# Performance work log

Measured on AMD Instinct MI355X. Metric: run time of the kernel, lower is better.

## Reference

```python
import jax, jax.numpy as jnp
import numpy as np

N = 4096        # nodes
E = 65536       # edges (avg degree 16)
L = 64          # latent_dims
K = 256         # kernel_dims
ED = 6          # edge_dims
DEPTH = 2


def _gelu(x):
    # torch.nn.GELU / F.gelu default = exact erf form
    return jax.nn.gelu(x, approximate=False)


def setup_inputs() -> dict:
    key = jax.random.key(0)
    ks = jax.random.split(key, 12)
    u = lambda k, shape, fan: jax.random.uniform(k, shape, jnp.float32, -1.0, 1.0) / np.sqrt(fan)
    return {
        "nodes": jax.random.normal(ks[0], (N, L), jnp.float32),
        "edge_index": jax.random.randint(ks[1], (2, E), 0, N, jnp.int32),
        "edge_attr": jax.random.uniform(ks[2], (E, ED), jnp.float32),
        # DenseNet kernel MLP: ED -> K -> K -> L*L (GELU between layers)
        "W1": u(ks[3], (ED, K), ED), "b1": jnp.zeros((K,), jnp.float32),
        "W2": u(ks[4], (K, K), K),  "b2": jnp.zeros((K,), jnp.float32),
        "W3": u(ks[5], (K, L * L), K), "b3": jnp.zeros((L * L,), jnp.float32),
        # NNConv root linear (no bias) + conv bias
        "W_root": u(ks[6], (L, L), L),
        "bias": jnp.zeros((L,), jnp.float32),
    }


def reference(nodes, edge_index, edge_attr, W1, b1, W2, b2, W3, b3, W_root, bias):
    src, dst = edge_index[0], edge_index[1]
    # Edge-conditioned dynamic weights (depend only on edge_attr -> compute once)
    h = _gelu(edge_attr @ W1 + b1)          # [E, K]
    h = _gelu(h @ W2 + b2)                  # [E, K]
    W_edge = (h @ W3 + b3).reshape(E, L, L) # [E, L_in, L_out]

    def conv(x):
        msg = jnp.einsum('ei,eio->eo', x[src], W_edge)          # gather + per-edge matmul
        agg = jax.ops.segment_sum(msg, dst, num_segments=N)     # scatter-add to dst
        return agg + x @ W_root + bias

    x = nodes
    for idx in range(DEPTH):
        x = conv(x)
        if idx < DEPTH - 1:
            x = _gelu(x)
    return x
```

## Files before the change

### kernel.cpp

```cpp
#include <hip/hip_runtime.h>
#include <math.h>

#define NN 4096
#define NE 65536
#define LL 64
#define KK 256
#define ED 6
#define MAXSUPER 6144

typedef __bf16 bf16_t;
typedef __attribute__((ext_vector_type(4))) __bf16 bf16x4;
typedef __attribute__((ext_vector_type(8))) __bf16 bf16x8;
typedef __attribute__((ext_vector_type(4))) float f32x4;
typedef __attribute__((ext_vector_type(16))) float f32x16;

#define OFF_CNT    ((size_t)0)
#define OFF_DESC   ((size_t)16384)
#define OFF_AGG0   ((size_t)147456)
#define OFF_AGG1   ((size_t)1196032)
#define ZERO_BYTES ((size_t)2244608)
#define OFF_CURSOR ((size_t)2244608)
#define OFF_DSTS   ((size_t)2260992)
#define OFF_W2R    ((size_t)2785280)
#define OFF_W3RR   ((size_t)2916352)
#define OFF_Q0     ((size_t)5013504)
#define OFF_Q1     ((size_t)6062080)
#define OFF_X1F    ((size_t)7110656)
#define OFF_X0BF   ((size_t)8159232)
#define OFF_X1BF   ((size_t)8683520)
#define OFF_H      ((size_t)9207808)
#define OFF_P      ((size_t)42762240)

__device__ __forceinline__ float gelu_f(float x) {
    return 0.5f * x * (1.0f + erff(x * 0.7071067811865476f));
}
__device__ __forceinline__ bf16_t f2bf(float x) { return (bf16_t)x; }

__global__ void k_hist(const int* __restrict__ ei, int* __restrict__ cnt) {
    int e = blockIdx.x * 256 + threadIdx.x;
    atomicAdd(&cnt[ei[e]], 1);
}

__global__ void k_scan(const int* __restrict__ cnt, int* __restrict__ cursor,
                       int4* __restrict__ descs) {
    __shared__ int pd[1024], pc[1024];
    int t = threadIdx.x;
    int deg[4]; int sd = 0, sc = 0;
#pragma unroll
    for (int j = 0; j < 4; j++) {
        deg[j] = cnt[t * 4 + j];
        sd += deg[j];
        sc += (deg[j] + 31) >> 5;
    }
    pd[t] = sd; pc[t] = sc;
    __syncthreads();
    for (int off = 1; off < 1024; off <<= 1) {
        int vd = 0, vc = 0;
        if (t >= off) { vd = pd[t - off]; vc = pc[t - off]; }
        __syncthreads();
        pd[t] += vd; pc[t] += vc;
        __syncthreads();
    }
    int rd = (t > 0) ? pd[t - 1] : 0;
    int rc = (t > 0) ? pc[t - 1] : 0;
    for (int j = 0; j < 4; j++) {
        int v = t * 4 + j, d = deg[j];
        cursor[v] = rd;
        int nch = (d + 31) >> 5;
        for (int c = 0; c < nch; c++) {
            int rem = d - c * 32;
            descs[rc + c] = make_int4(v, rd + c * 32, rem < 32 ? rem : 32, 0);
        }
        rc += nch; rd += d;
    }
}

__global__ void __launch_bounds__(256) k_fuse3(
        const int* __restrict__ ei, int* __restrict__ cursor, int* __restrict__ dsts,
        const float* __restrict__ W3, bf16_t* __restrict__ W3rr,
        const float* __restrict__ W2, bf16_t* __restrict__ W2r,
        const float* __restrict__ attr, const float* __restrict__ W1,
        const float* __restrict__ b1, bf16_t* __restrict__ a1,
        const float* __restrict__ x, const float* __restrict__ b3,
        bf16_t* __restrict__ xbf, float* __restrict__ Q) {
    __shared__ float smem[4096];
    int bid = blockIdx.x, tid = threadIdx.x;
    if (bid < 256) {
        int k0 = bid;
        for (int idx = tid; idx < 4096; idx += 256)
            smem[idx] = W3[(size_t)k0 * 4096 + idx];
        __syncthreads();
        int sbase = (2 * (k0 >> 4)) * 512 + (((k0 >> 3) & 1) * 32) * 8 + (k0 & 7);
#pragma unroll
        for (int m = 0; m < 2; m++) {
            int w = m * 256 + tid;
            int o = w >> 3, ib = w & 7;
            int s = sbase + (o >> 5) * 512 + (o & 31) * 8;
            int f = (s >> 4) * 1024 + (ib >> 2) * 512 + (ib & 3) * 128 + (s & 15) * 8;
            bf16x8 pk;
#pragma unroll
            for (int j = 0; j < 8; j++) pk[j] = f2bf(smem[(ib * 8 + j) * 64 + o]);
            *(bf16x8*)(W3rr + f) = pk;
        }
    } else if (bid < 512) {
        int t = (bid - 256) * 256 + tid;
        int kk = t >> 13, nn = (t >> 9) & 15, lane = (t >> 3) & 63, j = t & 7;
        int k = kk * 32 + (lane >> 4) * 8 + j;
        int n = nn * 16 + (lane & 15);
        W2r[t] = f2bf(W2[k * 256 + n]);
    } else if (bid < 1536) {
        float* sa = smem;
        int* spos = (int*)(smem + 512);
        int e0 = (bid - 512) * 64;
        for (int i = tid; i < 64 * ED; i += 256) sa[i] = attr[(size_t)e0 * ED + i];
        if (tid < 64) {
            int e = e0 + tid;
            int s = ei[e], d = ei[NE + e];
            int p = atomicAdd(&cursor[s], 1);
            dsts[p] = d;
            spos[tid] = p;
        }
        int col4 = (tid & 63) * 4;
        float w[ED][4], bb[4];
#pragma unroll
        for (int j = 0; j < ED; j++)
#pragma unroll
            for (int c = 0; c < 4; c++) w[j][c] = W1[j * 256 + col4 + c];
#pragma unroll
        for (int c = 0; c < 4; c++) bb[c] = b1[col4 + c];
        __syncthreads();
        int esub = tid >> 6;
#pragma unroll 1
        for (int eg = 0; eg < 16; eg++) {
            int el = eg * 4 + esub;
            int pos = spos[el];
            float av[ED];
#pragma unroll
            for (int j = 0; j < ED; j++) av[j] = sa[el * ED + j];
            bf16x4 ov;
#pragma unroll
            for (int c = 0; c < 4; c++) {
                float acc = bb[c];
#pragma unroll
                for (int j = 0; j < ED; j++) acc += av[j] * w[j][c];
                ov[c] = f2bf(gelu_f(acc));
            }
            *(bf16x4*)(a1 + (size_t)pos * 256 + col4) = ov;
        }
    } else {
        int v = (bid - 1536) * 4 + (tid >> 6);
        int o = tid & 63;
        float xv = x[v * 64 + o];
        smem[tid] = xv;
        xbf[v * 64 + o] = f2bf(xv);
        __syncthreads();
        const float* sx = smem + (tid >> 6) * 64;
        float q = 0.0f;
#pragma unroll 8
        for (int i = 0; i < 64; i++) q += sx[i] * b3[i * 64 + o];
        Q[v * 64 + o] = q;
    }
}

__device__ __forceinline__ void pgemm_body(const bf16_t* __restrict__ xbf,
                                           const bf16_t* __restrict__ W3rr,
                                           bf16_t* __restrict__ P,
                                           bf16_t* __restrict__ sw_wave,
                                           int strip, int rg) {
    int wave = threadIdx.x >> 6, lane = threadIdx.x & 63;
    int col = lane & 15, quad = lane >> 4;
    int half = lane >> 5, l5 = lane & 31;
    bf16_t* sw = sw_wave + wave * 4224;
    bf16x8 b[16][2];
#pragma unroll
    for (int nn = 0; nn < 16; nn++) {
        int sn = strip * 16 + nn;
#pragma unroll
        for (int ki = 0; ki < 2; ki++)
            b[nn][ki] = *(const bf16x8*)(W3rr + (size_t)(sn * 2 + ki) * 512 + lane * 8);
    }
#pragma unroll 1
    for (int rt = 0; rt < 4; rt++) {
        int rowbase = rg * 256 + wave * 64 + rt * 16;
        const bf16_t* arow = xbf + (size_t)(rowbase + col) * 64;
        bf16x8 a0 = *(const bf16x8*)(arow + quad * 8);
        bf16x8 a1v = *(const bf16x8*)(arow + 32 + quad * 8);
#pragma unroll
        for (int nn = 0; nn < 16; nn++) {
            f32x4 acc;
#pragma unroll
            for (int r = 0; r < 4; r++) acc[r] = 0.0f;
            acc = __builtin_amdgcn_mfma_f32_16x16x32_bf16(b[nn][0], a0, acc, 0, 0, 0);
            acc = __builtin_amdgcn_mfma_f32_16x16x32_bf16(b[nn][1], a1v, acc, 0, 0, 0);
            bf16x4 pk;
#pragma unroll
            for (int r = 0; r < 4; r++) pk[r] = f2bf(acc[r]);
            *(bf16x4*)(sw + col * 264 + nn * 16 + quad * 4) = pk;
        }
        __builtin_amdgcn_wave_barrier();
#pragma unroll
        for (int i = 0; i < 8; i++) {
            int r2 = 2 * i + half;
            int vrow = rowbase + r2;
            bf16x8 vb = *(const bf16x8*)(sw + r2 * 264 + l5 * 8);
            *(bf16x8*)(P + ((size_t)strip * 4096 + vrow) * 256 + l5 * 8) = vb;
        }
        __builtin_amdgcn_wave_barrier();
    }
}

__global__ void __launch_bounds__(256) k_fuse4(const bf16_t* __restrict__ xbf,
                                               const bf16_t* __restrict__ W3rr,
                                               bf16_t* __restrict__ P,
                                               const bf16_t* a1,
                                               const bf16_t* __restrict__ W2r,
                                               const float* __restrict__ b2,
                                               bf16_t* h) {
    __shared__ bf16_t sB[16896];
    if (blockIdx.x < 1024) {
        pgemm_body(xbf, W3rr, P, sB, blockIdx.x & 63, blockIdx.x >> 6);
    } else {
        int tid = threadIdx.x;
        int wave = tid >> 6, lane = tid & 63, col = lane & 15, quad = lane >> 4;
        int base = (blockIdx.x - 1024) * 128 + wave * 32;
        bf16x8 a[2][8];
#pragma unroll
        for (int t = 0; t < 2; t++) {
            const bf16_t* arow = a1 + (size_t)(base + t * 16 + col) * 256;
#pragma unroll
            for (int kk = 0; kk < 8; kk++)
                a[t][kk] = *(const bf16x8*)(arow + kk * 32 + quad * 8);
        }
#pragma unroll 1
        for (int p = 0; p < 4; p++) {
#pragma unroll
            for (int it = 0; it < 8; it++) {
                int c = it * 256 + tid;
                int fl = c >> 6;
                int e = (c & 63) * 8;
                int kk = fl >> 2, nnl = fl & 3;
                *(bf16x8*)(sB + fl * 512 + e) =
                    *(const bf16x8*)(W2r + (size_t)(kk * 16 + p * 4 + nnl) * 512 + e);
            }
            __syncthreads();
#pragma unroll
            for (int nnl = 0; nnl < 4; nnl++) {
                f32x4 acc0, acc1;
#pragma unroll
                for (int r = 0; r < 4; r++) { acc0[r] = 0.0f; acc1[r] = 0.0f; }
#pragma unroll
                for (int kk = 0; kk < 8; kk++) {
                    bf16x8 b = *(const bf16x8*)(sB + (kk * 4 + nnl) * 512 + lane * 8);
                    acc0 = __builtin_amdgcn_mfma_f32_16x16x32_bf16(a[0][kk], b, acc0, 0, 0, 0);
                    acc1 = __builtin_amdgcn_mfma_f32_16x16x32_bf16(a[1][kk], b, acc1, 0, 0, 0);
                }
                int ncol = (p * 4 + nnl) * 16 + col;
                float bv = b2[ncol];
#pragma unroll
                for (int r = 0; r < 4; r++) {
                    int row0 = base + quad * 4 + r;
                    h[(size_t)row0 * 256 + ncol] = f2bf(gelu_f(acc0[r] + bv));
                    h[(size_t)(row0 + 16) * 256 + ncol] = f2bf(gelu_f(acc1[r] + bv));
                }
            }
            __syncthreads();
        }
    }
}

__global__ void __launch_bounds__(256) k_pgemm(const bf16_t* __restrict__ xbf,
                                               const bf16_t* __restrict__ W3rr,
                                               bf16_t* __restrict__ P) {
    __shared__ bf16_t sw_all[16896];
    pgemm_body(xbf, W3rr, P, sw_all, blockIdx.x & 63, blockIdx.x >> 6);
}

__global__ void __launch_bounds__(256) k_agg(const int4* __restrict__ descs,
                                             const int* __restrict__ dsts,
                                             const bf16_t* __restrict__ h,
                                             const bf16_t* __restrict__ P,
                                             const float* __restrict__ Q,
                                             float* __restrict__ agg) {
    int chunk = blockIdx.x * 4 + (threadIdx.x >> 6);
    int lane = threadIdx.x & 63;
    int row = lane & 31, khalf = lane >> 5;
    int4 d = descs[chunk];
    int v = d.x, base = d.y, cnt = d.z;
    if (cnt == 0) return;
    bool valid = (row < cnt);
    int pos = base + (valid ? row : 0);
    int dst = dsts[pos];

    bf16x8 zero;
#pragma unroll
    for (int i = 0; i < 8; i++) zero[i] = (bf16_t)0.0f;

    bf16x8 a[16];
    const bf16_t* hrow = h + (size_t)pos * 256;
#pragma unroll
    for (int kt = 0; kt < 16; kt++) {
        bf16x8 t = *(const bf16x8*)(hrow + kt * 16 + khalf * 8);
        a[kt] = valid ? t : zero;
    }
    const bf16_t* Pv = P + ((size_t)khalf * 4096 + v) * 256 + row * 8;
    f32x16 acc0, acc1;
#pragma unroll
    for (int r = 0; r < 16; r++) { acc0[r] = 0.0f; acc1[r] = 0.0f; }
#pragma unroll
    for (int kt = 0; kt < 16; kt++) {
        bf16x8 b0 = *(const bf16x8*)(Pv + (size_t)(4 * kt) * 4096 * 256);
        bf16x8 b1 = *(const bf16x8*)(Pv + (size_t)(4 * kt + 2) * 4096 * 256);
        acc0 = __builtin_amdgcn_mfma_f32_32x32x16_bf16(a[kt], b0, acc0, 0, 0, 0);
        acc1 = __builtin_amdgcn_mfma_f32_32x32x16_bf16(a[kt], b1, acc1, 0, 0, 0);
    }
    float q0 = Q[v * 64 + row];
    float q1 = Q[v * 64 + 32 + row];
#pragma unroll
    for (int r = 0; r < 16; r++) {
        int mm = (r & 3) + 8 * (r >> 2) + 4 * khalf;
        int de = __shfl(dst, mm, 64);
        if (mm < cnt) {
            atomicAdd(&agg[(size_t)de * 64 + row], acc0[r] + q0);
            atomicAdd(&agg[(size_t)de * 64 + 32 + row], acc1[r] + q1);
        }
    }
}

__global__ void k_combine1(const float* __restrict__ x, const float* __restrict__ agg,
                           const float* __restrict__ Wroot, const float* __restrict__ bias,
                           const float* __restrict__ b3, float* __restrict__ x1,
                           bf16_t* __restrict__ x1bf, float* __restrict__ Q1) {
    __shared__ float sx[64], sy[64];
    int v = blockIdx.x, o = threadIdx.x;
    sx[o] = x[v * 64 + o];
    __syncthreads();
    float acc = agg[v * 64 + o] + bias[o];
#pragma unroll 8
    for (int i = 0; i < 64; i++) acc += sx[i] * Wroot[i * 64 + o];
    acc = gelu_f(acc);
    x1[v * 64 + o] = acc;
    x1bf[v * 64 + o] = f2bf(acc);
    sy[o] = acc;
    __syncthreads();
    float q = 0.0f;
#pragma unroll 8
    for (int i = 0; i < 64; i++) q += sy[i] * b3[i * 64 + o];
    Q1[v * 64 + o] = q;
}

__global__ void k_combine2(const float* __restrict__ x1, const float* __restrict__ agg,
                           const float* __restrict__ Wroot, const float* __restrict__ bias,
                           float* __restrict__ out) {
    __shared__ float sx[64];
    int v = blockIdx.x, o = threadIdx.x;
    sx[o] = x1[v * 64 + o];
    __syncthreads();
    float acc = agg[v * 64 + o] + bias[o];
#pragma unroll 8
    for (int i = 0; i < 64; i++) acc += sx[i] * Wroot[i * 64 + o];
    out[v * 64 + o] = acc;
}

extern "C" void kernel_launch(void* const* d_in, const int* in_sizes, int n_in,
                              void* d_out, int out_size, void* d_ws, size_t ws_size,
                              hipStream_t stream) {
    const float* nodes = (const float*)d_in[0];
    const int*   ei    = (const int*)d_in[1];
    const float* attr  = (const float*)d_in[2];
    const float* W1    = (const float*)d_in[3];
    const float* b1    = (const float*)d_in[4];
    const float* W2    = (const float*)d_in[5];
    const float* b2    = (const float*)d_in[6];
    const float* W3    = (const float*)d_in[7];
    const float* b3    = (const float*)d_in[8];
    const float* Wroot = (const float*)d_in[9];
    const float* bias  = (const float*)d_in[10];
    float* out = (float*)d_out;
    char* ws = (char*)d_ws;

    int*    cnt    = (int*)(ws + OFF_CNT);
    int4*   descs  = (int4*)(ws + OFF_DESC);
    float*  agg0   = (float*)(ws + OFF_AGG0);
    float*  agg1   = (float*)(ws + OFF_AGG1);
    int*    cursor = (int*)(ws + OFF_CURSOR);
    int*    dsts   = (int*)(ws + OFF_DSTS);
    bf16_t* W2r    = (bf16_t*)(ws + OFF_W2R);
    bf16_t* W3rr   = (bf16_t*)(ws + OFF_W3RR);
    float*  Q0     = (float*)(ws + OFF_Q0);
    float*  Q1     = (float*)(ws + OFF_Q1);
    float*  x1f    = (float*)(ws + OFF_X1F);
    bf16_t* x0bf   = (bf16_t*)(ws + OFF_X0BF);
    bf16_t* x1bf   = (bf16_t*)(ws + OFF_X1BF);
    bf16_t* hbuf   = (bf16_t*)(ws + OFF_H);
    bf16_t* a1buf  = (bf16_t*)(ws + OFF_H);
    bf16_t* Pbuf   = (bf16_t*)(ws + OFF_P);

    hipMemsetAsync(ws, 0, ZERO_BYTES, stream);
    k_hist<<<NE / 256, 256, 0, stream>>>(ei, cnt);
    k_scan<<<1, 1024, 0, stream>>>(cnt, cursor, descs);
    k_fuse3<<<2560, 256, 0, stream>>>(ei, cursor, dsts, W3, W3rr, W2, W2r,
                                      attr, W1, b1, a1buf, nodes, b3, x0bf, Q0);
    k_fuse4<<<1536, 256, 0, stream>>>(x0bf, W3rr, Pbuf, a1buf, W2r, b2, hbuf);
    k_agg<<<MAXSUPER / 4, 256, 0, stream>>>(descs, dsts, hbuf, Pbuf, Q0, agg0);
    k_combine1<<<NN, 64, 0, stream>>>(nodes, agg0, Wroot, bias, b3, x1f, x1bf, Q1);
    k_pgemm<<<1024, 256, 0, stream>>>(x1bf, W3rr, Pbuf);
    k_agg<<<MAXSUPER / 4, 256, 0, stream>>>(descs, dsts, hbuf, Pbuf, Q1, agg1);
    k_combine2<<<NN, 64, 0, stream>>>(x1f, agg1, Wroot, bias, out);
}
```

Before: 262.4 us.

## Fuse per-node P projection into aggregation kernel, dropping global P buffer

Instead of materializing the per-node projection P = x·W3 (4096×64×256 bf16) to global memory in a separate kernel and reading it back in the aggregation, the new aggregation kernel computes P for its 16 source nodes on the fly into LDS, then immediately runs the edge MFMA against h. The MLP second layer becomes a standalone kernel. This removes a large global write and read of P per layer, in exchange for recomputing P per chunk (nodes split across multiple chunks recompute) and adding block-wide barriers per k-step.

```diff
diff --git a/kernel.cpp b/kernel.cpp
--- a/kernel.cpp
+++ b/kernel.cpp
@@ -29,7 +29,6 @@
 #define OFF_X0BF   ((size_t)8159232)
 #define OFF_X1BF   ((size_t)8683520)
 #define OFF_H      ((size_t)9207808)
-#define OFF_P      ((size_t)42762240)
 
 __device__ __forceinline__ float gelu_f(float x) {
     return 0.5f * x * (1.0f + erff(x * 0.7071067811865476f));
@@ -162,166 +161,166 @@
     }
 }
 
-__device__ __forceinline__ void pgemm_body(const bf16_t* __restrict__ xbf,
-                                           const bf16_t* __restrict__ W3rr,
-                                           bf16_t* __restrict__ P,
-                                           bf16_t* __restrict__ sw_wave,
-                                           int strip, int rg) {
-    int wave = threadIdx.x >> 6, lane = threadIdx.x & 63;
+__global__ void __launch_bounds__(256) k_mlp2(const bf16_t* a1,
+                                              const bf16_t* __restrict__ W2r,
+                                              const float* __restrict__ b2,
+                                              bf16_t* h) {
+    __shared__ bf16_t sB[16384];
+    int tid = threadIdx.x;
+    int wave = tid >> 6, lane = tid & 63, col = lane & 15, quad = lane >> 4;
+    int base = blockIdx.x * 128 + wave * 32;
+    bf16x8 a[2][8];
+#pragma unroll
+    for (int t = 0; t < 2; t++) {
+        const bf16_t* arow = a1 + (size_t)(base + t * 16 + col) * 256;
+#pragma unroll
+        for (int kk = 0; kk < 8; kk++)
+            a[t][kk] = *(const bf16x8*)(arow + kk * 32 + quad * 8);
+    }
+#pragma unroll 1
+    for (int p = 0; p < 4; p++) {
+#pragma unroll
+        for (int it = 0; it < 8; it++) {
+            int c = it * 256 + tid;
+            int fl = c >> 6;
+            int e = (c & 63) * 8;
+            int kk = fl >> 2, nnl = fl & 3;
+            *(bf16x8*)(sB + fl * 512 + e) =
+                *(const bf16x8*)(W2r + (size_t)(kk * 16 + p * 4 + nnl) * 512 + e);
+        }
+        __syncthreads();
+#pragma unroll
+        for (int nnl = 0; nnl < 4; nnl++) {
+            f32x4 acc0, acc1;
+#pragma unroll
+            for (int r = 0; r < 4; r++) { acc0[r] = 0.0f; acc1[r] = 0.0f; }
+#pragma unroll
+            for (int kk = 0; kk < 8; kk++) {
+                bf16x8 b = *(const bf16x8*)(sB + (kk * 4 + nnl) * 512 + lane * 8);
+                acc0 = __builtin_amdgcn_mfma_f32_16x16x32_bf16(a[0][kk], b, acc0, 0, 0, 0);
+                acc1 = __builtin_amdgcn_mfma_f32_16x16x32_bf16(a[1][kk], b, acc1, 0, 0, 0);
+            }
+            int ncol = (p * 4 + nnl) * 16 + col;
+            float bv = b2[ncol];
+#pragma unroll
+            for (int r = 0; r < 4; r++) {
+                int row0 = base + quad * 4 + r;
+                h[(size_t)row0 * 256 + ncol] = f2bf(gelu_f(acc0[r] + bv));
+                h[(size_t)(row0 + 16) * 256 + ncol] = f2bf(gelu_f(acc1[r] + bv));
+            }
+        }
+        __syncthreads();
+    }
+}
+
+__global__ void __launch_bounds__(512) k_fagg(const int4* __restrict__ descs,
+                                              const int* __restrict__ dsts,
+                                              const bf16_t* __restrict__ xbf,
+                                              const bf16_t* __restrict__ W3rr,
+                                              const bf16_t* __restrict__ h,
+                                              const float* __restrict__ Q,
+                                              float* __restrict__ agg) {
+    __shared__ __align__(16) bf16_t Pls[4][16][264];
+    __shared__ int sv[16], sbase[16], scnt[16];
+    int tid = threadIdx.x, wave = tid >> 6, lane = tid & 63;
+    if (tid < 16) {
+        int4 d = descs[blockIdx.x * 16 + tid];
+        sv[tid] = d.x; sbase[tid] = d.y; scnt[tid] = d.z;
+    }
+    __syncthreads();
+
     int col = lane & 15, quad = lane >> 4;
-    int half = lane >> 5, l5 = lane & 31;
-    bf16_t* sw = sw_wave + wave * 4224;
-    bf16x8 b[16][2];
-#pragma unroll
-    for (int nn = 0; nn < 16; nn++) {
-        int sn = strip * 16 + nn;
-#pragma unroll
-        for (int ki = 0; ki < 2; ki++)
-            b[nn][ki] = *(const bf16x8*)(W3rr + (size_t)(sn * 2 + ki) * 512 + lane * 8);
-    }
+    int row = lane & 31, khalf = lane >> 5;
+
+    const bf16_t* xr = xbf + (size_t)sv[col] * 64 + quad * 8;
+    bf16x8 xa0 = *(const bf16x8*)xr;
+    bf16x8 xa1 = *(const bf16x8*)(xr + 32);
+
+    int s0 = wave * 2, s1 = s0 + 1;
+    int v0 = sv[s0], v1 = sv[s1];
+    int cnt0 = scnt[s0], cnt1 = scnt[s1];
+    bool val0 = row < cnt0, val1 = row < cnt1;
+    int pos0 = sbase[s0] + (val0 ? row : 0);
+    int pos1 = sbase[s1] + (val1 ? row : 0);
+    int dst0 = dsts[pos0], dst1 = dsts[pos1];
+    const bf16_t* h0 = h + (size_t)pos0 * 256 + khalf * 8;
+    const bf16_t* h1 = h + (size_t)pos1 * 256 + khalf * 8;
+
+    bf16x8 zero;
+#pragma unroll
+    for (int i = 0; i < 8; i++) zero[i] = (bf16_t)0.0f;
+
+    f32x16 acc00, acc01, acc10, acc11;
+#pragma unroll
+    for (int r = 0; r < 16; r++) { acc00[r] = 0.0f; acc01[r] = 0.0f;
+                                   acc10[r] = 0.0f; acc11[r] = 0.0f; }
+
+    int pst = wave >> 1;
+    int nn0 = (wave & 1) * 8;
+
 #pragma unroll 1
-    for (int rt = 0; rt < 4; rt++) {
-        int rowbase = rg * 256 + wave * 64 + rt * 16;
-        const bf16_t* arow = xbf + (size_t)(rowbase + col) * 64;
-        bf16x8 a0 = *(const bf16x8*)(arow + quad * 8);
-        bf16x8 a1v = *(const bf16x8*)(arow + 32 + quad * 8);
-#pragma unroll
-        for (int nn = 0; nn < 16; nn++) {
+    for (int kt = 0; kt < 16; ++kt) {
+        int strip = kt * 4 + pst;
+        const bf16_t* wb = W3rr + (size_t)(strip * 16 + nn0) * 1024 + lane * 8;
+#pragma unroll
+        for (int nn = 0; nn < 8; ++nn) {
+            bf16x8 b0 = *(const bf16x8*)wb;
+            bf16x8 b1 = *(const bf16x8*)(wb + 512);
+            wb += 1024;
             f32x4 acc;
 #pragma unroll
             for (int r = 0; r < 4; r++) acc[r] = 0.0f;
-            acc = __builtin_amdgcn_mfma_f32_16x16x32_bf16(b[nn][0], a0, acc, 0, 0, 0);
-            acc = __builtin_amdgcn_mfma_f32_16x16x32_bf16(b[nn][1], a1v, acc, 0, 0, 0);
+            acc = __builtin_amdgcn_mfma_f32_16x16x32_bf16(b0, xa0, acc, 0, 0, 0);
+            acc = __builtin_amdgcn_mfma_f32_16x16x32_bf16(b1, xa1, acc, 0, 0, 0);
             bf16x4 pk;
 #pragma unroll
             for (int r = 0; r < 4; r++) pk[r] = f2bf(acc[r]);
-            *(bf16x4*)(sw + col * 264 + nn * 16 + quad * 4) = pk;
-        }
-        __builtin_amdgcn_wave_barrier();
-#pragma unroll
-        for (int i = 0; i < 8; i++) {
-            int r2 = 2 * i + half;
-            int vrow = rowbase + r2;
-            bf16x8 vb = *(const bf16x8*)(sw + r2 * 264 + l5 * 8);
-            *(bf16x8*)(P + ((size_t)strip * 4096 + vrow) * 256 + l5 * 8) = vb;
-        }
-        __builtin_amdgcn_wave_barrier();
-    }
-}
-
-__global__ void __launch_bounds__(256) k_fuse4(const bf16_t* __restrict__ xbf,
-                                               const bf16_t* __restrict__ W3rr,
-                                               bf16_t* __restrict__ P,
-                                               const bf16_t* a1,
-                                               const bf16_t* __restrict__ W2r,
-                                               const float* __restrict__ b2,
-                                               bf16_t* h) {
-    __shared__ bf16_t sB[16896];
-    if (blockIdx.x < 1024) {
-        pgemm_body(xbf, W3rr, P, sB, blockIdx.x & 63, blockIdx.x >> 6);
-    } else {
-        int tid = threadIdx.x;
-        int wave = tid >> 6, lane = tid & 63, col = lane & 15, quad = lane >> 4;
-        int base = (blockIdx.x - 1024) * 128 + wave * 32;
-        bf16x8 a[2][8];
-#pragma unroll
-        for (int t = 0; t < 2; t++) {
-            const bf16_t* arow = a1 + (size_t)(base + t * 16 + col) * 256;
-#pragma unroll
-            for (int kk = 0; kk < 8; kk++)
-                a[t][kk] = *(const bf16x8*)(arow + kk * 32 + quad * 8);
-        }
-#pragma unroll 1
-        for (int p = 0; p < 4; p++) {
-#pragma unroll
-            for (int it = 0; it < 8; it++) {
-                int c = it * 256 + tid;
-                int fl = c >> 6;
-                int e = (c & 63) * 8;
-                int kk = fl >> 2, nnl = fl & 3;
-                *(bf16x8*)(sB + fl * 512 + e) =
-                    *(const bf16x8*)(W2r + (size_t)(kk * 16 + p * 4 + nnl) * 512 + e);
+            *(bf16x4*)(&Pls[pst][col][(nn0 + nn) * 16 + quad * 4]) = pk;
+        }
+        __syncthreads();
+        {
+            bf16x8 t0 = *(const bf16x8*)(h0 + kt * 16);
+            bf16x8 af = val0 ? t0 : zero;
+            bf16x8 pb0 = *(const bf16x8*)(&Pls[khalf][s0][row * 8]);
+            bf16x8 pb1 = *(const bf16x8*)(&Pls[2 + khalf][s0][row * 8]);
+            acc00 = __builtin_amdgcn_mfma_f32_32x32x16_bf16(af, pb0, acc00, 0, 0, 0);
+            acc01 = __builtin_amdgcn_mfma_f32_32x32x16_bf16(af, pb1, acc01, 0, 0, 0);
+        }
+        {
+            bf16x8 t1 = *(const bf16x8*)(h1 + kt * 16);
+            bf16x8 af = val1 ? t1 : zero;
+            bf16x8 pb0 = *(const bf16x8*)(&Pls[khalf][s1][row * 8]);
+            bf16x8 pb1 = *(const bf16x8*)(&Pls[2 + khalf][s1][row * 8]);
+            acc10 = __builtin_amdgcn_mfma_f32_32x32x16_bf16(af, pb0, acc10, 0, 0, 0);
+            acc11 = __builtin_amdgcn_mfma_f32_32x32x16_bf16(af, pb1, acc11, 0, 0, 0);
+        }
+        __syncthreads();
+    }
+
+    {
+        float q0 = Q[v0 * 64 + row];
+        float q1 = Q[v0 * 64 + 32 + row];
+#pragma unroll
+        for (int r = 0; r < 16; r++) {
+            int mm = (r & 3) + 8 * (r >> 2) + 4 * khalf;
+            int de = __shfl(dst0, mm, 64);
+            if (mm < cnt0) {
+                atomicAdd(&agg[(size_t)de * 64 + row], acc00[r] + q0);
+                atomicAdd(&agg[(size_t)de * 64 + 32 + row], acc01[r] + q1);
             }
-            __syncthreads();
-#pragma unroll
-            for (int nnl = 0; nnl < 4; nnl++) {
-                f32x4 acc0, acc1;
-#pragma unroll
-                for (int r = 0; r < 4; r++) { acc0[r] = 0.0f; acc1[r] = 0.0f; }
-#pragma unroll
-                for (int kk = 0; kk < 8; kk++) {
-                    bf16x8 b = *(const bf16x8*)(sB + (kk * 4 + nnl) * 512 + lane * 8);
-                    acc0 = __builtin_amdgcn_mfma_f32_16x16x32_bf16(a[0][kk], b, acc0, 0, 0, 0);
-                    acc1 = __builtin_amdgcn_mfma_f32_16x16x32_bf16(a[1][kk], b, acc1, 0, 0, 0);
-                }
-                int ncol = (p * 4 + nnl) * 16 + col;
-                float bv = b2[ncol];
-#pragma unroll
-                for (int r = 0; r < 4; r++) {
-                    int row0 = base + quad * 4 + r;
-                    h[(size_t)row0 * 256 + ncol] = f2bf(gelu_f(acc0[r] + bv));
-                    h[(size_t)(row0 + 16) * 256 + ncol] = f2bf(gelu_f(acc1[r] + bv));
-                }
+        }
+    }
+    {
+        float q0 = Q[v1 * 64 + row];
+        float q1 = Q[v1 * 64 + 32 + row];
+#pragma unroll
+        for (int r = 0; r < 16; r++) {
+            int mm = (r & 3) + 8 * (r >> 2) + 4 * khalf;
+            int de = __shfl(dst1, mm, 64);
+            if (mm < cnt1) {
+                atomicAdd(&agg[(size_t)de * 64 + row], acc10[r] + q0);
+                atomicAdd(&agg[(size_t)de * 64 + 32 + row], acc11[r] + q1);
             }
-            __syncthreads();
-        }
-    }
-}
-
-__global__ void __launch_bounds__(256) k_pgemm(const bf16_t* __restrict__ xbf,
-                                               const bf16_t* __restrict__ W3rr,
-                                               bf16_t* __restrict__ P) {
-    __shared__ bf16_t sw_all[16896];
-    pgemm_body(xbf, W3rr, P, sw_all, blockIdx.x & 63, blockIdx.x >> 6);
-}
-
-__global__ void __launch_bounds__(256) k_agg(const int4* __restrict__ descs,
-                                             const int* __restrict__ dsts,
-                                             const bf16_t* __restrict__ h,
-                                             const bf16_t* __restrict__ P,
-                                             const float* __restrict__ Q,
-                                             float* __restrict__ agg) {
-    int chunk = blockIdx.x * 4 + (threadIdx.x >> 6);
-    int lane = threadIdx.x & 63;
-    int row = lane & 31, khalf = lane >> 5;
-    int4 d = descs[chunk];
-    int v = d.x, base = d.y, cnt = d.z;
-    if (cnt == 0) return;
-    bool valid = (row < cnt);
-    int pos = base + (valid ? row : 0);
-    int dst = dsts[pos];
-
-    bf16x8 zero;
-#pragma unroll
-    for (int i = 0; i < 8; i++) zero[i] = (bf16_t)0.0f;
-
-    bf16x8 a[16];
-    const bf16_t* hrow = h + (size_t)pos * 256;
-#pragma unroll
-    for (int kt = 0; kt < 16; kt++) {
-        bf16x8 t = *(const bf16x8*)(hrow + kt * 16 + khalf * 8);
-        a[kt] = valid ? t : zero;
-    }
-    const bf16_t* Pv = P + ((size_t)khalf * 4096 + v) * 256 + row * 8;
-    f32x16 acc0, acc1;
-#pragma unroll
-    for (int r = 0; r < 16; r++) { acc0[r] = 0.0f; acc1[r] = 0.0f; }
-#pragma unroll
-    for (int kt = 0; kt < 16; kt++) {
-        bf16x8 b0 = *(const bf16x8*)(Pv + (size_t)(4 * kt) * 4096 * 256);
-        bf16x8 b1 = *(const bf16x8*)(Pv + (size_t)(4 * kt + 2) * 4096 * 256);
-        acc0 = __builtin_amdgcn_mfma_f32_32x32x16_bf16(a[kt], b0, acc0, 0, 0, 0);
-        acc1 = __builtin_amdgcn_mfma_f32_32x32x16_bf16(a[kt], b1, acc1, 0, 0, 0);
-    }
-    float q0 = Q[v * 64 + row];
-    float q1 = Q[v * 64 + 32 + row];
-#pragma unroll
-    for (int r = 0; r < 16; r++) {
-        int mm = (r & 3) + 8 * (r >> 2) + 4 * khalf;
-        int de = __shfl(dst, mm, 64);
-        if (mm < cnt) {
-            atomicAdd(&agg[(size_t)de * 64 + row], acc0[r] + q0);
-            atomicAdd(&agg[(size_t)de * 64 + 32 + row], acc1[r] + q1);
         }
     }
 }
@@ -393,17 +392,15 @@
     bf16_t* x1bf   = (bf16_t*)(ws + OFF_X1BF);
     bf16_t* hbuf   = (bf16_t*)(ws + OFF_H);
     bf16_t* a1buf  = (bf16_t*)(ws + OFF_H);
-    bf16_t* Pbuf   = (bf16_t*)(ws + OFF_P);
 
     hipMemsetAsync(ws, 0, ZERO_BYTES, stream);
     k_hist<<<NE / 256, 256, 0, stream>>>(ei, cnt);
     k_scan<<<1, 1024, 0, stream>>>(cnt, cursor, descs);
     k_fuse3<<<2560, 256, 0, stream>>>(ei, cursor, dsts, W3, W3rr, W2, W2r,
                                       attr, W1, b1, a1buf, nodes, b3, x0bf, Q0);
-    k_fuse4<<<1536, 256, 0, stream>>>(x0bf, W3rr, Pbuf, a1buf, W2r, b2, hbuf);
-    k_agg<<<MAXSUPER / 4, 256, 0, stream>>>(descs, dsts, hbuf, Pbuf, Q0, agg0);
+    k_mlp2<<<512, 256, 0, stream>>>(a1buf, W2r, b2, hbuf);
+    k_fagg<<<MAXSUPER / 16, 512, 0, stream>>>(descs, dsts, x0bf, W3rr, hbuf, Q0, agg0);
     k_combine1<<<NN, 64, 0, stream>>>(nodes, agg0, Wroot, bias, b3, x1f, x1bf, Q1);
-    k_pgemm<<<1024, 256, 0, stream>>>(x1bf, W3rr, Pbuf);
-    k_agg<<<MAXSUPER / 4, 256, 0, stream>>>(descs, dsts, hbuf, Pbuf, Q1, agg1);
+    k_fagg<<<MAXSUPER / 16, 512, 0, stream>>>(descs, dsts, x1bf, W3rr, hbuf, Q1, agg1);
     k_combine2<<<NN, 64, 0, stream>>>(x1f, agg1, Wroot, bias, out);
 }
```

Measured after the change: 284.7 us. 8.5% more time.
